# Optimization experiments

Hardware: AMD Instinct MI355X
Metric: run time of the kernel (lower is better)

The kernel has to match this reference:

```python
import jax, jax.numpy as jnp
import numpy as np

NHEAD = 16  # n_head; head_size N = C // NHEAD = 64


def _forward(x, time_maa_x, time_maa, time_maa_w1, time_maa_w2,
             time_decay, time_decay_w1, time_decay_w2,
             time_aaaaa, time_aaa_w1, time_aaa_w2,
             time_kkk_w1, time_kkk_w2,
             gate_w1, gate_w2,
             time_misc_a, ma_w1, ma_w2,
             time_misc_k, mk_w1, mk_w2,
             receptance, key_w, value, output,
             ln_w, ln_b, time_faaaa):
    B, T, C = x.shape
    H, N = NHEAD, C // NHEAD
    # --- fused_time_shift: token shift + 4-way LoRA mixing (rg, wa, k, v) ---
    xprev = jnp.pad(x, ((0, 0), (1, 0), (0, 0)))[:, :T]   # shift right by one token
    xx = xprev - x
    xxx = x + xx * time_maa_x
    mix = jnp.tanh(xxx @ time_maa_w1.T).reshape(B, T, 4, -1)        # (B,T,4,32)
    deltas = jnp.einsum('btfd,fcd->fbtc', mix, time_maa_w2)         # (4,B,T,C)
    xrg, xwa, xk, xv = x[None] + xx[None] * (time_maa + deltas)
    # --- projections + small LoRAs ---
    r = xrg @ receptance.T
    g = jnp.tanh(xrg @ gate_w1.T) @ gate_w2.T                       # gate
    k = xk @ key_w.T
    kk1 = jnp.tanh(xk @ time_kkk_w1.T)
    mk1 = xk @ mk_w1.T
    v = xv @ value.T
    w1 = jnp.tanh(xwa @ time_decay_w1.T)
    a1 = xwa @ time_aaa_w1.T
    ma1 = xwa @ ma_w1.T
    # data-dependent log-decay, clamped <= -0.5 via softplus
    w = -jax.nn.softplus(-(time_decay + w1 @ time_decay_w2.T)) - 0.5
    # removal key kk: per-head L2-normalized
    kk = k + kk1 @ time_kkk_w2.T
    kk = kk.reshape(B, T, H, N)
    kk = kk / jnp.maximum(jnp.linalg.norm(kk, axis=-1, keepdims=True), 1e-12)
    kk = kk.reshape(B, T, C)
    a = jax.nn.sigmoid(time_aaaaa + a1 @ time_aaa_w2.T)
    ma = jax.nn.sigmoid(time_misc_a + ma1 @ ma_w2.T)
    k = k * ma + k * a * (1 - ma)
    mk = jax.nn.sigmoid(time_misc_k + mk1 @ mk_w2.T)
    k = k * jnp.exp(w * mk)
    b = -kk * a
    # --- RWKV-7 linear-attention scan; state S: (B,H,N_value,N_key) ---
    def heads(z):
        return z.reshape(B, T, H, N).transpose(1, 0, 2, 3)          # (T,B,H,N)
    rh, wh, kh, vh, kkh, bh = map(heads, (r, w, k, v, kk, b))

    def step(S, inp):
        r_, w_, k_, v_, kk_, b_ = inp
        sab = jnp.einsum('bhvk,bhk->bhv', S, kk_)                   # S @ kk
        S = (S * jnp.exp(w_)[:, :, None, :]                         # diag decay on key dim
             + sab[..., None] * b_[:, :, None, :]                   # (S kk) b^T  (delta-rule removal)
             + v_[..., None] * k_[:, :, None, :])                   # v k^T
        y = jnp.einsum('bhvk,bhk->bhv', S, r_)
        return S, y

    S0 = jnp.zeros((B, H, N, N), x.dtype)
    _, y = jax.lax.scan(step, S0, (rh, wh, kh, vh, kkh, bh))
    y = y.transpose(1, 0, 2, 3)                                     # (B,T,H,N)
    # --- GroupNorm (H groups, eps=64e-5) + r.k bonus + gate (fused_attn_ln tail) ---
    mu = y.mean(-1, keepdims=True)
    var = ((y - mu) ** 2).mean(-1, keepdims=True)
    yn = (y - mu) / jnp.sqrt(var + 0.00064) * ln_w.reshape(H, N) + ln_b.reshape(H, N)
    r4 = r.reshape(B, T, H, N)
    k4 = k.reshape(B, T, H, N)
    v4 = v.reshape(B, T, H, N)
    bonus = (r4 * k4 * time_faaaa.reshape(H, N)).sum(-1, keepdims=True) * v4
    out = (yn + bonus).reshape(B, T, C) * g
    return out @ output.T


def setup_inputs() -> dict:
    key = jax.random.key(0)
    ks = iter(jax.random.split(key, 40))
    B, T, C = 2, 1024, 1024
    def n(shape, s=1.0):
        return jax.random.normal(next(ks), shape, jnp.float32) * s
    def u(shape, lo, hi):
        return jax.random.uniform(next(ks), shape, jnp.float32, lo, hi)
    d = {}
    d['x'] = n((B, T, C))
    d['time_maa_x'] = u((1, 1, C), 0.0, 1.0)
    d['time_maa'] = u((4, 1, 1, C), 0.0, 1.0)
    d['time_maa_w1'] = n((128, C), 0.02)
    d['time_maa_w2'] = n((4, C, 32), 0.05)
    d['time_decay'] = u((1, 1, C), -6.5, -1.5)
    d['time_decay_w1'] = n((64, C), 0.02)
    d['time_decay_w2'] = n((C, 64), 0.05)
    d['time_aaaaa'] = n((1, 1, C), 0.1)
    d['time_aaa_w1'] = n((16, C), 0.02)
    d['time_aaa_w2'] = n((C, 16), 0.05)
    d['time_kkk_w1'] = n((16, C), 0.02)
    d['time_kkk_w2'] = n((C, 16), 0.05)
    d['gate_w1'] = n((128, C), 0.05)
    d['gate_w2'] = n((C, 128), 0.05)
    d['time_misc_a'] = n((1, 1, C), 0.1)
    d['ma_w1'] = n((16, C), 0.02)
    d['ma_w2'] = n((C, 16), 0.05)
    d['time_misc_k'] = n((1, 1, C), 0.1)
    d['mk_w1'] = n((16, C), 0.02)
    d['mk_w2'] = n((C, 16), 0.05)
    s = 0.5 / C ** 0.5
    d['receptance'] = u((C, C), -s, s)
    d['key_w'] = u((C, C), -0.1 * s, 0.1 * s)
    d['value'] = u((C, C), -s, s)
    d['output'] = n((C, C), 0.02)
    d['ln_w'] = jnp.ones((C,), jnp.float32)
    d['ln_b'] = jnp.zeros((C,), jnp.float32)
    d['time_faaaa'] = n((C,), 0.1)
    return d


def reference(x, time_maa_x, time_maa, time_maa_w1, time_maa_w2,
              time_decay, time_decay_w1, time_decay_w2,
              time_aaaaa, time_aaa_w1, time_aaa_w2,
              time_kkk_w1, time_kkk_w2,
              gate_w1, gate_w2,
              time_misc_a, ma_w1, ma_w2,
              time_misc_k, mk_w1, mk_w2,
              receptance, key_w, value, output,
              ln_w, ln_b, time_faaaa):
    return _forward(x, time_maa_x, time_maa, time_maa_w1, time_maa_w2,
                    time_decay, time_decay_w1, time_decay_w2,
                    time_aaaaa, time_aaa_w1, time_aaa_w2,
                    time_kkk_w1, time_kkk_w2,
                    gate_w1, gate_w2,
                    time_misc_a, ma_w1, ma_w2,
                    time_misc_k, mk_w1, mk_w2,
                    receptance, key_w, value, output,
                    ln_w, ln_b, time_faaaa)
```

## Files before the change

kernel.cpp:

```cpp
#include <hip/hip_runtime.h>
#include <hip/hip_bf16.h>

typedef __hip_bfloat16 bf16;

#define B_ 2
#define T_ 1024
#define C_ 1024
#define H_ 16
#define N_ 64

using short4v = __attribute__((ext_vector_type(4))) short;
using short8 = __attribute__((ext_vector_type(8))) short;
using f32x4 = __attribute__((ext_vector_type(4))) float;

__device__ __forceinline__ float bs2f(short s) {
  return __uint_as_float(((unsigned int)(unsigned short)s) << 16);
}
__device__ __forceinline__ bf16 f2bf(float f) { return __float2bfloat16(f); }
__device__ __forceinline__ short bfbits(float f) {
  bf16 h = __float2bfloat16(f);
  return *reinterpret_cast<short*>(&h);
}
__device__ __forceinline__ float sigmoidf_(float x) { return 1.0f / (1.0f + expf(-x)); }
__device__ __forceinline__ float softplusf_(float x) {
  return fmaxf(x, 0.0f) + log1pf(expf(-fabsf(x)));
}
__device__ __forceinline__ void gload16(const bf16* g, bf16* l) {
  __builtin_amdgcn_global_load_lds(
      (const __attribute__((address_space(1))) unsigned int*)g,
      (__attribute__((address_space(3))) unsigned int*)l, 16, 0, 0);
}
__device__ __forceinline__ float qsum16(float x) {
  int a = __builtin_amdgcn_update_dpp(0, __float_as_int(x), 0xB1, 0xF, 0xF, true);
  x += __int_as_float(a);
  int b = __builtin_amdgcn_update_dpp(0, __float_as_int(x), 0x4E, 0xF, 0xF, true);
  x += __int_as_float(b);
  int c = __builtin_amdgcn_update_dpp(0, __float_as_int(x), 0x124, 0xF, 0xF, true);
  x += __int_as_float(c);
  int d = __builtin_amdgcn_update_dpp(0, __float_as_int(x), 0x128, 0xF, 0xF, true);
  x += __int_as_float(d);
  return x;
}
__device__ __forceinline__ void qsum16x2(float& x, float& y) {
  int a0 = __builtin_amdgcn_update_dpp(0, __float_as_int(x), 0xB1, 0xF, 0xF, true);
  int b0 = __builtin_amdgcn_update_dpp(0, __float_as_int(y), 0xB1, 0xF, 0xF, true);
  x += __int_as_float(a0); y += __int_as_float(b0);
  int a1 = __builtin_amdgcn_update_dpp(0, __float_as_int(x), 0x4E, 0xF, 0xF, true);
  int b1 = __builtin_amdgcn_update_dpp(0, __float_as_int(y), 0x4E, 0xF, 0xF, true);
  x += __int_as_float(a1); y += __int_as_float(b1);
  int a2 = __builtin_amdgcn_update_dpp(0, __float_as_int(x), 0x124, 0xF, 0xF, true);
  int b2 = __builtin_amdgcn_update_dpp(0, __float_as_int(y), 0x124, 0xF, 0xF, true);
  x += __int_as_float(a2); y += __int_as_float(b2);
  int a3 = __builtin_amdgcn_update_dpp(0, __float_as_int(x), 0x128, 0xF, 0xF, true);
  int b3 = __builtin_amdgcn_update_dpp(0, __float_as_int(y), 0x128, 0xF, 0xF, true);
  x += __int_as_float(a3); y += __int_as_float(b3);
}

__global__ __launch_bounds__(256) void cvt_mix_kernel(
    const float* __restrict__ s0, const float* __restrict__ s1,
    const float* __restrict__ s2, const float* __restrict__ s3,
    const float* __restrict__ s4, const float* __restrict__ s5,
    const float* __restrict__ s6,
    bf16* __restrict__ d0, bf16* __restrict__ d1, bf16* __restrict__ d2w,
    bf16* __restrict__ d3, bf16* __restrict__ d4, bf16* __restrict__ d5,
    bf16* __restrict__ d6,
    const float* __restrict__ tkw1, const float* __restrict__ mkw1,
    const float* __restrict__ tdw1, const float* __restrict__ taw1,
    const float* __restrict__ maw1,
    bf16* __restrict__ wsk, bf16* __restrict__ wswa,
    const float* __restrict__ tmw2, const float* __restrict__ tdw2,
    const float* __restrict__ tkw2, const float* __restrict__ taw2,
    const float* __restrict__ maw2, const float* __restrict__ mkw2,
    bf16* __restrict__ tmw2e, bf16* __restrict__ w2e5,
    const float* __restrict__ x, const float* __restrict__ tmx,
    bf16* __restrict__ mixb) {
  long bidx = blockIdx.x;
  if (bidx >= 5760) {
    __shared__ __align__(16) bf16 As[128][72];
    __shared__ __align__(16) bf16 Ws[64][72];
    const int K = 1024;
    int mb = (int)(bidx - 5760);
    int n0 = (mb & 1) << 6;
    int m0 = (mb >> 1) << 7;
    int tid = threadIdx.x;
    int arow = tid >> 1, acol = (tid & 1) << 5;
    int wrow = tid >> 2, wcol = (tid & 3) << 4;
    int wv = tid >> 6, lane = tid & 63;
    int fr = lane & 15, fq = lane >> 4;
    int grow = m0 + arow;
    int t = grow & (T_ - 1);
    const float* xp = x + (long)grow * C_ + acol;
    const float* Wp = s0 + (long)(n0 + wrow) * K + wcol;
    f32x4 a00 = {0.f, 0.f, 0.f, 0.f};
    f32x4 a01 = a00, a02 = a00, a03 = a00, a10 = a00, a11 = a00, a12 = a00, a13 = a00;
    for (int k0 = 0; k0 < K; k0 += 64) {
#pragma unroll
      for (int jj = 0; jj < 4; jj++) {
        int co = k0 + (jj << 3);
        float4 c0 = *(const float4*)(xp + co);
        float4 c1 = *(const float4*)(xp + co + 4);
        float4 q0 = {0.f, 0.f, 0.f, 0.f}, q1 = q0;
        if (t > 0) {
          q0 = *(const float4*)(xp + co - C_);
          q1 = *(const float4*)(xp + co + 4 - C_);
        }
        float4 m0v = *(const float4*)(tmx + co + acol);
        float4 m1v = *(const float4*)(tmx + co + acol + 4);
        short8 sv;
        sv[0] = bfbits(fmaf(q0.x - c0.x, m0v.x, c0.x));
        sv[1] = bfbits(fmaf(q0.y - c0.y, m0v.y, c0.y));
        sv[2] = bfbits(fmaf(q0.z - c0.z, m0v.z, c0.z));
        sv[3] = bfbits(fmaf(q0.w - c0.w, m0v.w, c0.w));
        sv[4] = bfbits(fmaf(q1.x - c1.x, m1v.x, c1.x));
        sv[5] = bfbits(fmaf(q1.y - c1.y, m1v.y, c1.y));
        sv[6] = bfbits(fmaf(q1.z - c1.z, m1v.z, c1.z));
        sv[7] = bfbits(fmaf(q1.w - c1.w, m1v.w, c1.w));
        *(short8*)&As[arow][acol + (jj << 3)] = sv;
      }
      {
        float4 w0 = *(const float4*)(Wp + k0);
        float4 w1 = *(const float4*)(Wp + k0 + 4);
        float4 w2 = *(const float4*)(Wp + k0 + 8);
        float4 w3 = *(const float4*)(Wp + k0 + 12);
        short8 wv0, wv1;
        wv0[0] = bfbits(w0.x); wv0[1] = bfbits(w0.y); wv0[2] = bfbits(w0.z); wv0[3] = bfbits(w0.w);
        wv0[4] = bfbits(w1.x); wv0[5] = bfbits(w1.y); wv0[6] = bfbits(w1.z); wv0[7] = bfbits(w1.w);
        wv1[0] = bfbits(w2.x); wv1[1] = bfbits(w2.y); wv1[2] = bfbits(w2.z); wv1[3] = bfbits(w2.w);
        wv1[4] = bfbits(w3.x); wv1[5] = bfbits(w3.y); wv1[6] = bfbits(w3.z); wv1[7] = bfbits(w3.w);
        *(short8*)&Ws[wrow][wcol] = wv0;
        *(short8*)&Ws[wrow][wcol + 8] = wv1;
      }
      __syncthreads();
#pragma unroll
      for (int kk = 0; kk < 2; kk++) {
        int ko = (fq << 3) + (kk << 5);
        short8 af0 = *(const short8*)&As[(wv << 5) + fr][ko];
        short8 af1 = *(const short8*)&As[(wv << 5) + 16 + fr][ko];
        short8 b0 = *(const short8*)&Ws[fr][ko];
        short8 b1 = *(const short8*)&Ws[16 + fr][ko];
        short8 b2 = *(const short8*)&Ws[32 + fr][ko];
        short8 b3 = *(const short8*)&Ws[48 + fr][ko];
        a00 = __builtin_amdgcn_mfma_f32_16x16x32_bf16(af0, b0, a00, 0, 0, 0);
        a01 = __builtin_amdgcn_mfma_f32_16x16x32_bf16(af0, b1, a01, 0, 0, 0);
        a02 = __builtin_amdgcn_mfma_f32_16x16x32_bf16(af0, b2, a02, 0, 0, 0);
        a03 = __builtin_amdgcn_mfma_f32_16x16x32_bf16(af0, b3, a03, 0, 0, 0);
        a10 = __builtin_amdgcn_mfma_f32_16x16x32_bf16(af1, b0, a10, 0, 0, 0);
        a11 = __builtin_amdgcn_mfma_f32_16x16x32_bf16(af1, b1, a11, 0, 0, 0);
        a12 = __builtin_amdgcn_mfma_f32_16x16x32_bf16(af1, b2, a12, 0, 0, 0);
        a13 = __builtin_amdgcn_mfma_f32_16x16x32_bf16(af1, b3, a13, 0, 0, 0);
      }
      __syncthreads();
    }
    const int Nz = 128;
    int ocol = n0 + fr;
    int orow0 = m0 + (wv << 5) + (fq << 2);
#define WRM(accv, mf, nt) { int col = ocol + ((nt) << 4); \
    _Pragma("unroll") for (int r = 0; r < 4; r++) { \
      long oi = (long)(orow0 + ((mf) << 4) + r) * Nz + col; \
      mixb[oi] = f2bf(tanhf(accv[r])); } }
    WRM(a00, 0, 0) WRM(a01, 0, 1) WRM(a02, 0, 2) WRM(a03, 0, 3)
    WRM(a10, 1, 0) WRM(a11, 1, 1) WRM(a12, 1, 2) WRM(a13, 1, 3)
#undef WRM
    return;
  }
  const float* s; bf16* d; long off;
  if (bidx < 4480) {
    long i4 = bidx * 256 + threadIdx.x;
    if (i4 < 32768) { s = s0; d = d0; off = i4; }
    else if (i4 < 294912) { s = s1; d = d1; off = i4 - 32768; }
    else if (i4 < 327680) { s = s2; d = d2w; off = i4 - 294912; }
    else if (i4 < 360448) { s = s3; d = d3; off = i4 - 327680; }
    else if (i4 < 622592) { s = s4; d = d4; off = i4 - 360448; }
    else if (i4 < 884736) { s = s5; d = d5; off = i4 - 622592; }
    else { s = s6; d = d6; off = i4 - 884736; }
  } else if (bidx < 4608) {
    long i4 = (bidx - 4480) * 256 + threadIdx.x;
    long so, dof;
    if (i4 < 4096) { s = tkw1; so = i4; d = wsk; dof = i4; }
    else if (i4 < 8192) { s = mkw1; so = i4 - 4096; d = wsk; dof = i4; }
    else if (i4 < 24576) { s = tdw1; so = i4 - 8192; d = wswa; dof = i4 - 8192; }
    else if (i4 < 28672) { s = taw1; so = i4 - 24576; d = wswa; dof = i4 - 8192; }
    else { s = maw1; so = i4 - 28672; d = wswa; dof = i4 - 8192; }
    float4 v = *(const float4*)(s + so * 4);
    d[dof * 4 + 0] = f2bf(v.x); d[dof * 4 + 1] = f2bf(v.y);
    d[dof * 4 + 2] = f2bf(v.z); d[dof * 4 + 3] = f2bf(v.w);
    return;
  } else if (bidx < 5120) {
    long i4 = (bidx - 4608) * 256 + threadIdx.x;
    long n = i4 >> 5;
    int k0 = (int)(i4 & 31) << 2;
    int f = (int)(n >> 10);
    float4 v = {0.f, 0.f, 0.f, 0.f};
    if ((k0 >> 5) == f) v = *(const float4*)(tmw2 + n * 32 + (k0 & 31));
    tmw2e[i4 * 4 + 0] = f2bf(v.x);
    tmw2e[i4 * 4 + 1] = f2bf(v.y);
    tmw2e[i4 * 4 + 2] = f2bf(v.z);
    tmw2e[i4 * 4 + 3] = f2bf(v.w);
    return;
  } else {
    long i4 = (bidx - 5120) * 256 + threadIdx.x;
    long rowi = i4 >> 5;
    int k0 = (int)(i4 & 31) << 2;
    int j = (int)(rowi >> 10);
    int c = (int)(rowi & 1023);
    float4 v = {0.f, 0.f, 0.f, 0.f};
    if (j == 0) { if (k0 < 64) v = *(const float4*)(tdw2 + c * 64 + k0); }
    else if (j == 1) { if (k0 >= 64 && k0 < 80) v = *(const float4*)(taw2 + c * 16 + (k0 - 64)); }
    else if (j == 2) { if (k0 >= 80 && k0 < 96) v = *(const float4*)(maw2 + c * 16 + (k0 - 80)); }
    else if (j == 3) { if (k0 >= 96 && k0 < 112) v = *(const float4*)(tkw2 + c * 16 + (k0 - 96)); }
    else { if (k0 >= 112) v = *(const float4*)(mkw2 + c * 16 + (k0 - 112)); }
    w2e5[i4 * 4 + 0] = f2bf(v.x);
    w2e5[i4 * 4 + 1] = f2bf(v.y);
    w2e5[i4 * 4 + 2] = f2bf(v.z);
    w2e5[i4 * 4 + 3] = f2bf(v.w);
    return;
  }
  float4 v = *(const float4*)(s + off * 4);
  d[off * 4 + 0] = f2bf(v.x);
  d[off * 4 + 1] = f2bf(v.y);
  d[off * 4 + 2] = f2bf(v.z);
  d[off * 4 + 3] = f2bf(v.w);
}

struct GemmBatch {
  const bf16* A[6]; const bf16* W[6];
  float* Cf[6]; bf16* Cb[6];
  int N[6]; int actN[6]; int ldc[6]; int coff[6];
};

__global__ __launch_bounds__(256) void gemm_batch_kernel(GemmBatch gb, int K) {
  __shared__ __align__(16) bf16 As[128][64];
  __shared__ __align__(16) bf16 Ws[64][64];
  int z = blockIdx.z;
  int Nz = gb.N[z];
  int n0 = blockIdx.x << 6;
  if (n0 >= Nz) return;
  int m0 = blockIdx.y << 7;
  int actN = gb.actN[z];
  int ldc = gb.ldc[z], coff = gb.coff[z];
  const bf16* A = gb.A[z];
  const bf16* W = gb.W[z];
  float* Cf = gb.Cf[z];
  bf16* Cb = gb.Cb[z];
  int tid = threadIdx.x;
  int wrow = tid >> 2, wcol = (tid & 3) << 4;
  int wv = tid >> 6, lane = tid & 63;
  int fr = lane & 15, fq = lane >> 4;
  int lrow = lane >> 3, lcol = (lane & 7) << 3;
  bool wok = (n0 + wrow) < Nz;
  bool fullW = (n0 + 64 <= Nz);
  const bf16* Ag = A + (long)m0 * K;
  const bf16* Wg = W + (long)n0 * K;
  const bf16* Wp = W + (long)(n0 + wrow) * K + wcol;
  short8 zz = {0, 0, 0, 0, 0, 0, 0, 0};
  f32x4 a00 = {0.f, 0.f, 0.f, 0.f};
  f32x4 a01 = a00, a02 = a00, a03 = a00, a10 = a00, a11 = a00, a12 = a00, a13 = a00;
  for (int k0 = 0; k0 < K; k0 += 64) {
#pragma unroll
    for (int i = 0; i < 4; i++) {
      int rb = (wv << 5) + (i << 3);
      gload16(Ag + (long)(rb + lrow) * K + k0 + lcol, &As[rb][0]);
    }
    if (fullW) {
#pragma unroll
      for (int i = 0; i < 2; i++) {
        int rb = (wv << 4) + (i << 3);
        gload16(Wg + (long)(rb + lrow) * K + k0 + lcol, &Ws[rb][0]);
      }
    } else {
      *(short8*)&Ws[wrow][wcol] = wok ? *(const short8*)(Wp + k0) : zz;
      *(short8*)&Ws[wrow][wcol + 8] = wok ? *(const short8*)(Wp + k0 + 8) : zz;
    }
    __syncthreads();
#pragma unroll
    for (int kk = 0; kk < 2; kk++) {
      int ko = (fq << 3) + (kk << 5);
      short8 af0 = *(const short8*)&As[(wv << 5) + fr][ko];
      short8 af1 = *(const short8*)&As[(wv << 5) + 16 + fr][ko];
      short8 b0 = *(const short8*)&Ws[fr][ko];
      short8 b1 = *(const short8*)&Ws[16 + fr][ko];
      short8 b2 = *(const short8*)&Ws[32 + fr][ko];
      short8 b3 = *(const short8*)&Ws[48 + fr][ko];
      a00 = __builtin_amdgcn_mfma_f32_16x16x32_bf16(af0, b0, a00, 0, 0, 0);
      a01 = __builtin_amdgcn_mfma_f32_16x16x32_bf16(af0, b1, a01, 0, 0, 0);
      a02 = __builtin_amdgcn_mfma_f32_16x16x32_bf16(af0, b2, a02, 0, 0, 0);
      a03 = __builtin_amdgcn_mfma_f32_16x16x32_bf16(af0, b3, a03, 0, 0, 0);
      a10 = __builtin_amdgcn_mfma_f32_16x16x32_bf16(af1, b0, a10, 0, 0, 0);
      a11 = __builtin_amdgcn_mfma_f32_16x16x32_bf16(af1, b1, a11, 0, 0, 0);
      a12 = __builtin_amdgcn_mfma_f32_16x16x32_bf16(af1, b2, a12, 0, 0, 0);
      a13 = __builtin_amdgcn_mfma_f32_16x16x32_bf16(af1, b3, a13, 0, 0, 0);
    }
    __syncthreads();
  }
  int ocol = n0 + fr;
  int orow0 = m0 + (wv << 5) + (fq << 2);
#define WRB(accv, mf, nt) { int col = ocol + ((nt) << 4); if (col < Nz) { \
    _Pragma("unroll") for (int r = 0; r < 4; r++) { \
      float vvv = accv[r]; if (col < actN) vvv = tanhf(vvv); \
      long oi = (long)(orow0 + ((mf) << 4) + r) * ldc + coff + col; \
      if (Cb) Cb[oi] = f2bf(vvv); else Cf[oi] = vvv; } } }
  WRB(a00, 0, 0) WRB(a01, 0, 1) WRB(a02, 0, 2) WRB(a03, 0, 3)
  WRB(a10, 1, 0) WRB(a11, 1, 1) WRB(a12, 1, 2) WRB(a13, 1, 3)
#undef WRB
}

__global__ __launch_bounds__(256) void gemm_mixapply_kernel(
    const bf16* __restrict__ A, const bf16* __restrict__ W,
    const float* __restrict__ x, const float* __restrict__ tmaa,
    bf16* __restrict__ xrg, bf16* __restrict__ xwa,
    bf16* __restrict__ xk, bf16* __restrict__ xv) {
  __shared__ __align__(16) bf16 As[128][64];
  __shared__ __align__(16) bf16 Ws[64][64];
  const int K = 128;
  int n0 = blockIdx.x << 6;
  int m0 = blockIdx.y << 7;
  int tid = threadIdx.x;
  int wv = tid >> 6, lane = tid & 63;
  int fr = lane & 15, fq = lane >> 4;
  int lrow = lane >> 3, lcol = (lane & 7) << 3;
  const bf16* Ag = A + (long)m0 * K;
  const bf16* Wg = W + (long)n0 * K;
  f32x4 a00 = {0.f, 0.f, 0.f, 0.f};
  f32x4 a01 = a00, a02 = a00, a03 = a00, a10 = a00, a11 = a00, a12 = a00, a13 = a00;
  for (int k0 = 0; k0 < K; k0 += 64) {
#pragma unroll
    for (int i = 0; i < 4; i++) {
      int rb = (wv << 5) + (i << 3);
      gload16(Ag + (long)(rb + lrow) * K + k0 + lcol, &As[rb][0]);
    }
#pragma unroll
    for (int i = 0; i < 2; i++) {
      int rb = (wv << 4) + (i << 3);
      gload16(Wg + (long)(rb + lrow) * K + k0 + lcol, &Ws[rb][0]);
    }
    __syncthreads();
#pragma unroll
    for (int kk = 0; kk < 2; kk++) {
      int ko = (fq << 3) + (kk << 5);
      short8 af0 = *(const short8*)&As[(wv << 5) + fr][ko];
      short8 af1 = *(const short8*)&As[(wv << 5) + 16 + fr][ko];
      short8 b0 = *(const short8*)&Ws[fr][ko];
      short8 b1 = *(const short8*)&Ws[16 + fr][ko];
      short8 b2 = *(const short8*)&Ws[32 + fr][ko];
      short8 b3 = *(const short8*)&Ws[48 + fr][ko];
      a00 = __builtin_amdgcn_mfma_f32_16x16x32_bf16(af0, b0, a00, 0, 0, 0);
      a01 = __builtin_amdgcn_mfma_f32_16x16x32_bf16(af0, b1, a01, 0, 0, 0);
      a02 = __builtin_amdgcn_mfma_f32_16x16x32_bf16(af0, b2, a02, 0, 0, 0);
      a03 = __builtin_amdgcn_mfma_f32_16x16x32_bf16(af0, b3, a03, 0, 0, 0);
      a10 = __builtin_amdgcn_mfma_f32_16x16x32_bf16(af1, b0, a10, 0, 0, 0);
      a11 = __builtin_amdgcn_mfma_f32_16x16x32_bf16(af1, b1, a11, 0, 0, 0);
      a12 = __builtin_amdgcn_mfma_f32_16x16x32_bf16(af1, b2, a12, 0, 0, 0);
      a13 = __builtin_amdgcn_mfma_f32_16x16x32_bf16(af1, b3, a13, 0, 0, 0);
    }
    __syncthreads();
  }
  int f = n0 >> 10;
  int c0 = n0 & 1023;
  bf16* outp = (f == 0) ? xrg : (f == 1) ? xwa : (f == 2) ? xk : xv;
  int ocol = c0 + fr;
  int orow0 = m0 + (wv << 5) + (fq << 2);
#define WRA(accv, mf, nt) { int cc = ocol + ((nt) << 4); \
    float ta = tmaa[(f << 10) + cc]; \
    _Pragma("unroll") for (int r = 0; r < 4; r++) { \
      int row = orow0 + ((mf) << 4) + r; \
      int t = row & (T_ - 1); \
      long xo = (long)row * C_ + cc; \
      float xb = x[xo]; \
      float xq = (t > 0) ? x[xo - C_] : 0.0f; \
      outp[xo] = f2bf(fmaf(xq - xb, ta + accv[r], xb)); } }
  WRA(a00, 0, 0) WRA(a01, 0, 1) WRA(a02, 0, 2) WRA(a03, 0, 3)
  WRA(a10, 1, 0) WRA(a11, 1, 1) WRA(a12, 1, 2) WRA(a13, 1, 3)
#undef WRA
}

__global__ __launch_bounds__(256) void fuse2_kernel(
    const float* __restrict__ kraw, const float* __restrict__ d2,
    const float* __restrict__ tdec, const float* __restrict__ taa,
    const float* __restrict__ tma, const float* __restrict__ tmk,
    float* __restrict__ ew, float* __restrict__ kfin,
    float* __restrict__ kkn, float* __restrict__ bbo) {
  int m = blockIdx.x, tid = threadIdx.x;
  int c4 = tid << 2;
  const float* dp = d2 + (long)m * 5120;
  float4 wd4 = *(const float4*)(dp + c4);
  float4 ad4 = *(const float4*)(dp + 1024 + c4);
  float4 mad4 = *(const float4*)(dp + 2048 + c4);
  float4 kd4 = *(const float4*)(dp + 3072 + c4);
  float4 mkd4 = *(const float4*)(dp + 4096 + c4);
  float4 kraw4 = *(const float4*)(kraw + (long)m * C_ + c4);
  float4 tdec4 = *(const float4*)(tdec + c4);
  float4 taa4 = *(const float4*)(taa + c4);
  float4 tma4 = *(const float4*)(tma + c4);
  float4 tmk4 = *(const float4*)(tmk + c4);
  float wd[4] = {wd4.x, wd4.y, wd4.z, wd4.w};
  float ad[4] = {ad4.x, ad4.y, ad4.z, ad4.w};
  float mad[4] = {mad4.x, mad4.y, mad4.z, mad4.w};
  float kd[4] = {kd4.x, kd4.y, kd4.z, kd4.w};
  float mkd[4] = {mkd4.x, mkd4.y, mkd4.z, mkd4.w};
  float krw[4] = {kraw4.x, kraw4.y, kraw4.z, kraw4.w};
  float td[4] = {tdec4.x, tdec4.y, tdec4.z, tdec4.w};
  float ta[4] = {taa4.x, taa4.y, taa4.z, taa4.w};
  float tm[4] = {tma4.x, tma4.y, tma4.z, tma4.w};
  float tk[4] = {tmk4.x, tmk4.y, tmk4.z, tmk4.w};
  float kkp[4], av[4], wvv[4], kr[4], mkv[4];
  float sumsq = 0.f;
#pragma unroll
  for (int j = 0; j < 4; j++) {
    float w = -softplusf_(-(td[j] + wd[j])) - 0.5f;
    wvv[j] = w;
    float kkpre = krw[j] + kd[j];
    kkp[j] = kkpre;
    sumsq += kkpre * kkpre;
    float a = sigmoidf_(ta[j] + ad[j]);
    av[j] = a;
    float ma = sigmoidf_(tm[j] + mad[j]);
    float mk = sigmoidf_(tk[j] + mkd[j]);
    mkv[j] = mk;
    kr[j] = krw[j] * (ma + a * (1.f - ma));
  }
  sumsq += __shfl_xor(sumsq, 1);
  sumsq += __shfl_xor(sumsq, 2);
  sumsq += __shfl_xor(sumsq, 4);
  sumsq += __shfl_xor(sumsq, 8);
  float rn = 1.0f / fmaxf(sqrtf(sumsq), 1e-12f);
  float4 kknv, bbov, eww, kfv;
  float* kknp = (float*)&kknv;
  float* bbop = (float*)&bbov;
  float* ewp = (float*)&eww;
  float* kfp = (float*)&kfv;
#pragma unroll
  for (int j = 0; j < 4; j++) {
    float kkx = kkp[j] * rn;
    kknp[j] = kkx;
    bbop[j] = -kkx * av[j];
    ewp[j] = expf(wvv[j]);
    kfp[j] = kr[j] * expf(wvv[j] * mkv[j]);
  }
  long off4 = (long)m * C_ + c4;
  *(float4*)(kkn + off4) = kknv;
  *(float4*)(bbo + off4) = bbov;
  *(float4*)(ew + off4) = eww;
  *(float4*)(kfin + off4) = kfv;
}

#define SCHUNK 16
#define NCHUNK (T_ / SCHUNK)
__global__ __launch_bounds__(256, 1) void scan_kernel(
    const float* __restrict__ rB, const float* __restrict__ ewB,
    const float* __restrict__ kB, const float* __restrict__ vB,
    const float* __restrict__ kkB, const float* __restrict__ bbB,
    float* __restrict__ yB) {
  __shared__ __align__(16) float lds[2][6][SCHUNK * 64];
  int bid = blockIdx.x;
  int bh = bid >> 2, rg = bid & 3;
  int b = bh >> 4, h = bh & 15;
  int tid = threadIdx.x;
  int wave = tid >> 6, lane = tid & 63;
  int g = lane >> 4, q = lane & 15;
  int row = (rg << 4) + (wave << 2) + g;
  int kq = q << 2;
  const long base = ((long)b * T_) * C_ + (h << 6);
  const float* s0 = kkB + base;
  const float* s1 = ewB + base;
  const float* s2 = kB + base;
  const float* s3 = bbB + base;
  const float* s4 = rB + base;
  const float* s5 = vB + base;
  int stok = tid >> 4;
  int spc = (tid & 15) << 2;
  int lo = (stok << 6) + spc;
  float4 rb0, rb1, rb2, rb3, rb4, rb5;
  auto loadc = [&](int c) {
    long go = (long)((c << 4) + stok) * C_ + spc;
    rb0 = *(const float4*)(s0 + go);
    rb1 = *(const float4*)(s1 + go);
    rb2 = *(const float4*)(s2 + go);
    rb3 = *(const float4*)(s3 + go);
    rb4 = *(const float4*)(s4 + go);
    rb5 = *(const float4*)(s5 + go);
  };
  auto stage = [&](int buf) {
    *(float4*)&lds[buf][0][lo] = rb0;
    *(float4*)&lds[buf][1][lo] = rb1;
    *(float4*)&lds[buf][2][lo] = rb2;
    *(float4*)&lds[buf][3][lo] = rb3;
    *(float4*)&lds[buf][4][lo] = rb4;
    *(float4*)&lds[buf][5][lo] = rb5;
  };
  float S0 = 0.f, S1 = 0.f, S2 = 0.f, S3 = 0.f;
  float ypv = 0.f;
  float4 Q0kk, Q0ew, Q0k, Q0bb, Q0r; float Q0v;
  float4 Q1kk, Q1ew, Q1k, Q1bb, Q1r; float Q1v;
  float4 Q2kk, Q2ew, Q2k, Q2bb, Q2r; float Q2v;

#define PF(i, tt) { int tb_ = ((tt) << 6); \
    Q##i##kk = *(const float4*)&lds[cur][0][tb_ + kq]; \
    Q##i##ew = *(const float4*)&lds[cur][1][tb_ + kq]; \
    Q##i##k  = *(const float4*)&lds[cur][2][tb_ + kq]; \
    Q##i##bb = *(const float4*)&lds[cur][3][tb_ + kq]; \
    Q##i##r  = *(const float4*)&lds[cur][4][tb_ + kq]; \
    Q##i##v  = lds[cur][5][tb_ + row]; }
#define SBAR __builtin_amdgcn_sched_barrier(0x7)
#define ST(i, gtok, FIRSTT) { \
    float p_ = fmaf(S1, Q##i##kk.y, S0 * Q##i##kk.x) + \
               fmaf(S3, Q##i##kk.w, S2 * Q##i##kk.z); \
    float yo_ = ypv; \
    qsum16x2(p_, yo_); \
    if (q == 0 && !((FIRSTT) && c == 0)) \
      yB[base + (long)((gtok) - 1) * C_ + row] = yo_; \
    float n0 = fmaf(S0, Q##i##ew.x, Q##i##v * Q##i##k.x); \
    float n1 = fmaf(S1, Q##i##ew.y, Q##i##v * Q##i##k.y); \
    float n2 = fmaf(S2, Q##i##ew.z, Q##i##v * Q##i##k.z); \
    float n3 = fmaf(S3, Q##i##ew.w, Q##i##v * Q##i##k.w); \
    S0 = fmaf(p_, Q##i##bb.x, n0); \
    S1 = fmaf(p_, Q##i##bb.y, n1); \
    S2 = fmaf(p_, Q##i##bb.z, n2); \
    S3 = fmaf(p_, Q##i##bb.w, n3); \
    ypv = fmaf(S1, Q##i##r.y, S0 * Q##i##r.x) + \
          fmaf(S3, Q##i##r.w, S2 * Q##i##r.z); }

  loadc(0);
  stage(0);
  loadc(1);
  __syncthreads();
  int cur = 0;
  for (int c = 0; c < NCHUNK; c++) {
    int t0 = c << 4;
    PF(0, 0); PF(1, 1);
    if (c + 1 < NCHUNK) stage(cur ^ 1);
    if (c + 2 < NCHUNK) loadc(c + 2);
    SBAR;
    PF(2, 2);  SBAR; ST(0, t0 + 0, true);
    PF(0, 3);  SBAR; ST(1, t0 + 1, false);
    PF(1, 4);  SBAR; ST(2, t0 + 2, false);
    PF(2, 5);  SBAR; ST(0, t0 + 3, false);
    PF(0, 6);  SBAR; ST(1, t0 + 4, false);
    PF(1, 7);  SBAR; ST(2, t0 + 5, false);
    PF(2, 8);  SBAR; ST(0, t0 + 6, false);
    PF(0, 9);  SBAR; ST(1, t0 + 7, false);
    PF(1, 10); SBAR; ST(2, t0 + 8, false);
    PF(2, 11); SBAR; ST(0, t0 + 9, false);
    PF(0, 12); SBAR; ST(1, t0 + 10, false);
    PF(1, 13); SBAR; ST(2, t0 + 11, false);
    PF(2, 14); SBAR; ST(0, t0 + 12, false);
    PF(0, 15); SBAR; ST(1, t0 + 13, false);
    ST(2, t0 + 14, false);
    ST(0, t0 + 15, false);
    __syncthreads();
    cur ^= 1;
  }
  {
    float yo = qsum16(ypv);
    if (q == 0) yB[base + (long)(T_ - 1) * C_ + row] = yo;
  }
#undef PF
#undef SBAR
#undef ST
}

__global__ __launch_bounds__(256) void gnout_kernel(
    const float* __restrict__ y, const float* __restrict__ r,
    const float* __restrict__ kf, const float* __restrict__ v,
    const float* __restrict__ g,
    const float* __restrict__ lnw, const float* __restrict__ lnb,
    const float* __restrict__ fa, bf16* __restrict__ z) {
  int tid = threadIdx.x;
  int w = tid >> 6, lane = tid & 63;
  int gi = (blockIdx.x << 2) + w;
  int h = gi & 15, mt = gi >> 4;
  long off = (long)mt * C_ + (h << 6) + lane;
  float yv = y[off];
  float s = yv;
  s += __shfl_xor(s, 1); s += __shfl_xor(s, 2); s += __shfl_xor(s, 4);
  s += __shfl_xor(s, 8); s += __shfl_xor(s, 16); s += __shfl_xor(s, 32);
  float mu = s * (1.0f / 64.0f);
  float d = yv - mu;
  float s2 = d * d;
  s2 += __shfl_xor(s2, 1); s2 += __shfl_xor(s2, 2); s2 += __shfl_xor(s2, 4);
  s2 += __shfl_xor(s2, 8); s2 += __shfl_xor(s2, 16); s2 += __shfl_xor(s2, 32);
  float var = s2 * (1.0f / 64.0f);
  int hc = (h << 6) + lane;
  float dot = r[off] * kf[off] * fa[hc];
  dot += __shfl_xor(dot, 1); dot += __shfl_xor(dot, 2); dot += __shfl_xor(dot, 4);
  dot += __shfl_xor(dot, 8); dot += __shfl_xor(dot, 16); dot += __shfl_xor(dot, 32);
  float yn = d * rsqrtf(var + 0.00064f) * lnw[hc] + lnb[hc];
  z[off] = f2bf((yn + dot * v[off]) * g[off]);
}

extern "C" void kernel_launch(void* const* d_in, const int* in_sizes, int n_in,
                              void* d_out, int out_size, void* d_ws, size_t ws_size,
                              hipStream_t stream) {
  const float* x = (const float*)d_in[0];
  const float* tmx = (const float*)d_in[1];
  const float* tmaa = (const float*)d_in[2];
  const float* tmw1 = (const float*)d_in[3];
  const float* tmw2 = (const float*)d_in[4];
  const float* tdec = (const float*)d_in[5];
  const float* tdw1 = (const float*)d_in[6];
  const float* tdw2 = (const float*)d_in[7];
  const float* taa5 = (const float*)d_in[8];
  const float* taw1 = (const float*)d_in[9];
  const float* taw2 = (const float*)d_in[10];
  const float* tkw1 = (const float*)d_in[11];
  const float* tkw2 = (const float*)d_in[12];
  const float* gw1 = (const float*)d_in[13];
  const float* gw2 = (const float*)d_in[14];
  const float* tmia = (const float*)d_in[15];
  const float* maw1 = (const float*)d_in[16];
  const float* maw2 = (const float*)d_in[17];
  const float* tmik = (const float*)d_in[18];
  const float* mkw1 = (const float*)d_in[19];
  const float* mkw2 = (const float*)d_in[20];
  const float* wrec = (const float*)d_in[21];
  const float* wkey = (const float*)d_in[22];
  const float* wval = (const float*)d_in[23];
  const float* wout = (const float*)d_in[24];
  const float* lnw = (const float*)d_in[25];
  const float* lnb = (const float*)d_in[26];
  const float* faaa = (const float*)d_in[27];

  const long MT = 2048, CC = 1024;
  char* base = (char*)d_ws;
  float* y = (float*)base;     base += MT * CC * 4;
  bf16* xrgb = (bf16*)base;    base += MT * CC * 2;
  bf16* xwab = (bf16*)base;    base += MT * CC * 2;
  bf16* xkb = (bf16*)base;     base += MT * CC * 2;
  bf16* xvb = (bf16*)base;     base += MT * CC * 2;
  float* rr = (float*)base;    base += MT * CC * 4;
  float* kraw = (float*)base;  base += MT * CC * 4;
  float* vv = (float*)base;    base += MT * CC * 4;
  float* gg = (float*)base;    base += MT * CC * 4;
  float* bbo = (float*)base;   base += MT * CC * 4;
  bf16* g1b = (bf16*)base;     base += MT * 128 * 2;
  bf16* out12b = (bf16*)base;  base += MT * 128 * 2;
  bf16* zb = (bf16*)base;      base += MT * CC * 2;
  bf16* mixb = (bf16*)base;    base += MT * 128 * 2;
  float* d2 = (float*)base;    base += MT * 5120L * 4;
  bf16* tmw1b = (bf16*)base;   base += 128 * CC * 2;
  bf16* wrecb = (bf16*)base;   base += CC * CC * 2;
  bf16* gw1b = (bf16*)base;    base += 128 * CC * 2;
  bf16* gw2b = (bf16*)base;    base += CC * 128 * 2;
  bf16* wkeyb = (bf16*)base;   base += CC * CC * 2;
  bf16* wvalb = (bf16*)base;   base += CC * CC * 2;
  bf16* woutb = (bf16*)base;   base += CC * CC * 2;
  bf16* wskb = (bf16*)base;    base += 32 * CC * 2;
  bf16* wswab = (bf16*)base;   base += 96 * CC * 2;
  bf16* tmw2e = (bf16*)base;   base += 4096L * 128 * 2;
  bf16* w2e5b = (bf16*)base;   base += 5120L * 128 * 2;
  float* ew = kraw;
  float* kfin = (float*)xrgb;
  float* kkn = (float*)xkb;

  cvt_mix_kernel<<<5792, 256, 0, stream>>>(
      tmw1, wrec, gw1, gw2, wkey, wval, wout,
      tmw1b, wrecb, gw1b, gw2b, wkeyb, wvalb, woutb,
      tkw1, mkw1, tdw1, taw1, maw1, wskb, wswab,
      tmw2, tdw2, tkw2, taw2, maw2, mkw2,
      tmw2e, w2e5b, x, tmx, mixb);

  gemm_mixapply_kernel<<<dim3(64, 16), 256, 0, stream>>>(
      mixb, tmw2e, x, tmaa, xrgb, xwab, xkb, xvb);
  {
    GemmBatch gb = {};
    gb.A[0] = xrgb; gb.W[0] = wrecb; gb.Cf[0] = rr;      gb.Cb[0] = nullptr; gb.N[0] = 1024; gb.actN[0] = 0;   gb.ldc[0] = 1024; gb.coff[0] = 0;
    gb.A[1] = xrgb; gb.W[1] = gw1b;  gb.Cf[1] = nullptr; gb.Cb[1] = g1b;     gb.N[1] = 128;  gb.actN[1] = 128; gb.ldc[1] = 128;  gb.coff[1] = 0;
    gb.A[2] = xkb;  gb.W[2] = wkeyb; gb.Cf[2] = kraw;    gb.Cb[2] = nullptr; gb.N[2] = 1024; gb.actN[2] = 0;   gb.ldc[2] = 1024; gb.coff[2] = 0;
    gb.A[3] = xkb;  gb.W[3] = wskb;  gb.Cf[3] = nullptr; gb.Cb[3] = out12b;  gb.N[3] = 32;   gb.actN[3] = 16;  gb.ldc[3] = 128;  gb.coff[3] = 96;
    gb.A[4] = xvb;  gb.W[4] = wvalb; gb.Cf[4] = vv;      gb.Cb[4] = nullptr; gb.N[4] = 1024; gb.actN[4] = 0;   gb.ldc[4] = 1024; gb.coff[4] = 0;
    gb.A[5] = xwab; gb.W[5] = wswab; gb.Cf[5] = nullptr; gb.Cb[5] = out12b;  gb.N[5] = 96;   gb.actN[5] = 64;  gb.ldc[5] = 128;  gb.coff[5] = 0;
    gemm_batch_kernel<<<dim3(16, 16, 6), 256, 0, stream>>>(gb, 1024);
  }
  {
    GemmBatch gb = {};
    gb.A[0] = g1b;    gb.W[0] = gw2b;  gb.Cf[0] = gg; gb.Cb[0] = nullptr; gb.N[0] = 1024; gb.actN[0] = 0; gb.ldc[0] = 1024; gb.coff[0] = 0;
    gb.A[1] = out12b; gb.W[1] = w2e5b; gb.Cf[1] = d2; gb.Cb[1] = nullptr; gb.N[1] = 5120; gb.actN[1] = 0; gb.ldc[1] = 5120; gb.coff[1] = 0;
    gemm_batch_kernel<<<dim3(80, 16, 2), 256, 0, stream>>>(gb, 128);
  }
  fuse2_kernel<<<2048, 256, 0, stream>>>(kraw, d2, tdec, taa5, tmia, tmik,
                                         ew, kfin, kkn, bbo);
  scan_kernel<<<128, 256, 0, stream>>>(rr, ew, kfin, vv, kkn, bbo, y);
  gnout_kernel<<<8192, 256, 0, stream>>>(y, rr, kfin, vv, gg, lnw, lnb, faaa, zb);
  {
    GemmBatch gb = {};
    gb.A[0] = zb; gb.W[0] = woutb; gb.Cf[0] = (float*)d_out; gb.Cb[0] = nullptr;
    gb.N[0] = 1024; gb.actN[0] = 0; gb.ldc[0] = 1024; gb.coff[0] = 0;
    gemm_batch_kernel<<<dim3(16, 16, 1), 256, 0, stream>>>(gb, 1024);
  }
}
```

Baseline: 423.4 us.

## Merge mid-pipeline GEMMs and fuse2 into one persistent cooperative kernel

Turns the mix-apply GEMM, the batched projection GEMMs, the LoRA second-stage GEMMs and the fuse2 elementwise pass into device functions. A single cooperative kernel walks over virtual block indices for each stage, with grid.sync between stages. The aim is to remove kernel launch gaps and tail idle time between the four launches. In exchange, it adds grid-wide barriers, caps the grid at occupancy×256 persistent blocks, and replaces the former z-indexed batching with an explicit tile-index map.

```diff
diff --git a/kernel.cpp b/kernel.cpp
--- a/kernel.cpp
+++ b/kernel.cpp
@@ -1,5 +1,8 @@
 #include <hip/hip_runtime.h>
 #include <hip/hip_bf16.h>
+#include <hip/hip_cooperative_groups.h>
+
+namespace cg = cooperative_groups;
 
 typedef __hip_bfloat16 bf16;
 
@@ -222,26 +225,10 @@
   d[off * 4 + 3] = f2bf(v.w);
 }
 
-struct GemmBatch {
-  const bf16* A[6]; const bf16* W[6];
-  float* Cf[6]; bf16* Cb[6];
-  int N[6]; int actN[6]; int ldc[6]; int coff[6];
-};
-
-__global__ __launch_bounds__(256) void gemm_batch_kernel(GemmBatch gb, int K) {
-  __shared__ __align__(16) bf16 As[128][64];
-  __shared__ __align__(16) bf16 Ws[64][64];
-  int z = blockIdx.z;
-  int Nz = gb.N[z];
-  int n0 = blockIdx.x << 6;
-  if (n0 >= Nz) return;
-  int m0 = blockIdx.y << 7;
-  int actN = gb.actN[z];
-  int ldc = gb.ldc[z], coff = gb.coff[z];
-  const bf16* A = gb.A[z];
-  const bf16* W = gb.W[z];
-  float* Cf = gb.Cf[z];
-  bf16* Cb = gb.Cb[z];
+__device__ __forceinline__ void gemm_tile(
+    const bf16* __restrict__ A, const bf16* __restrict__ W,
+    float* Cf, bf16* Cb, int Nz, int actN, int ldc, int coff, int K,
+    int n0, int m0, bf16* As, bf16* Ws) {
   int tid = threadIdx.x;
   int wrow = tid >> 2, wcol = (tid & 3) << 4;
   int wv = tid >> 6, lane = tid & 63;
@@ -259,28 +246,28 @@
 #pragma unroll
     for (int i = 0; i < 4; i++) {
       int rb = (wv << 5) + (i << 3);
-      gload16(Ag + (long)(rb + lrow) * K + k0 + lcol, &As[rb][0]);
+      gload16(Ag + (long)(rb + lrow) * K + k0 + lcol, As + rb * 64);
     }
     if (fullW) {
 #pragma unroll
       for (int i = 0; i < 2; i++) {
         int rb = (wv << 4) + (i << 3);
-        gload16(Wg + (long)(rb + lrow) * K + k0 + lcol, &Ws[rb][0]);
+        gload16(Wg + (long)(rb + lrow) * K + k0 + lcol, Ws + rb * 64);
       }
     } else {
-      *(short8*)&Ws[wrow][wcol] = wok ? *(const short8*)(Wp + k0) : zz;
-      *(short8*)&Ws[wrow][wcol + 8] = wok ? *(const short8*)(Wp + k0 + 8) : zz;
+      *(short8*)(Ws + wrow * 64 + wcol) = wok ? *(const short8*)(Wp + k0) : zz;
+      *(short8*)(Ws + wrow * 64 + wcol + 8) = wok ? *(const short8*)(Wp + k0 + 8) : zz;
     }
     __syncthreads();
 #pragma unroll
     for (int kk = 0; kk < 2; kk++) {
       int ko = (fq << 3) + (kk << 5);
-      short8 af0 = *(const short8*)&As[(wv << 5) + fr][ko];
-      short8 af1 = *(const short8*)&As[(wv << 5) + 16 + fr][ko];
-      short8 b0 = *(const short8*)&Ws[fr][ko];
-      short8 b1 = *(const short8*)&Ws[16 + fr][ko];
-      short8 b2 = *(const short8*)&Ws[32 + fr][ko];
-      short8 b3 = *(const short8*)&Ws[48 + fr][ko];
+      short8 af0 = *(const short8*)(As + ((wv << 5) + fr) * 64 + ko);
+      short8 af1 = *(const short8*)(As + ((wv << 5) + 16 + fr) * 64 + ko);
+      short8 b0 = *(const short8*)(Ws + fr * 64 + ko);
+      short8 b1 = *(const short8*)(Ws + (16 + fr) * 64 + ko);
+      short8 b2 = *(const short8*)(Ws + (32 + fr) * 64 + ko);
+      short8 b3 = *(const short8*)(Ws + (48 + fr) * 64 + ko);
       a00 = __builtin_amdgcn_mfma_f32_16x16x32_bf16(af0, b0, a00, 0, 0, 0);
       a01 = __builtin_amdgcn_mfma_f32_16x16x32_bf16(af0, b1, a01, 0, 0, 0);
       a02 = __builtin_amdgcn_mfma_f32_16x16x32_bf16(af0, b2, a02, 0, 0, 0);
@@ -304,16 +291,12 @@
 #undef WRB
 }
 
-__global__ __launch_bounds__(256) void gemm_mixapply_kernel(
+__device__ __forceinline__ void mixapply_tile(
     const bf16* __restrict__ A, const bf16* __restrict__ W,
     const float* __restrict__ x, const float* __restrict__ tmaa,
-    bf16* __restrict__ xrg, bf16* __restrict__ xwa,
-    bf16* __restrict__ xk, bf16* __restrict__ xv) {
-  __shared__ __align__(16) bf16 As[128][64];
-  __shared__ __align__(16) bf16 Ws[64][64];
+    bf16* xrg, bf16* xwa, bf16* xk, bf16* xv,
+    int n0, int m0, bf16* As, bf16* Ws) {
   const int K = 128;
-  int n0 = blockIdx.x << 6;
-  int m0 = blockIdx.y << 7;
   int tid = threadIdx.x;
   int wv = tid >> 6, lane = tid & 63;
   int fr = lane & 15, fq = lane >> 4;
@@ -326,23 +309,23 @@
 #pragma unroll
     for (int i = 0; i < 4; i++) {
       int rb = (wv << 5) + (i << 3);
-      gload16(Ag + (long)(rb + lrow) * K + k0 + lcol, &As[rb][0]);
+      gload16(Ag + (long)(rb + lrow) * K + k0 + lcol, As + rb * 64);
     }
 #pragma unroll
     for (int i = 0; i < 2; i++) {
       int rb = (wv << 4) + (i << 3);
-      gload16(Wg + (long)(rb + lrow) * K + k0 + lcol, &Ws[rb][0]);
+      gload16(Wg + (long)(rb + lrow) * K + k0 + lcol, Ws + rb * 64);
     }
     __syncthreads();
 #pragma unroll
     for (int kk = 0; kk < 2; kk++) {
       int ko = (fq << 3) + (kk << 5);
-      short8 af0 = *(const short8*)&As[(wv << 5) + fr][ko];
-      short8 af1 = *(const short8*)&As[(wv << 5) + 16 + fr][ko];
-      short8 b0 = *(const short8*)&Ws[fr][ko];
-      short8 b1 = *(const short8*)&Ws[16 + fr][ko];
-      short8 b2 = *(const short8*)&Ws[32 + fr][ko];
-      short8 b3 = *(const short8*)&Ws[48 + fr][ko];
+      short8 af0 = *(const short8*)(As + ((wv << 5) + fr) * 64 + ko);
+      short8 af1 = *(const short8*)(As + ((wv << 5) + 16 + fr) * 64 + ko);
+      short8 b0 = *(const short8*)(Ws + fr * 64 + ko);
+      short8 b1 = *(const short8*)(Ws + (16 + fr) * 64 + ko);
+      short8 b2 = *(const short8*)(Ws + (32 + fr) * 64 + ko);
+      short8 b3 = *(const short8*)(Ws + (48 + fr) * 64 + ko);
       a00 = __builtin_amdgcn_mfma_f32_16x16x32_bf16(af0, b0, a00, 0, 0, 0);
       a01 = __builtin_amdgcn_mfma_f32_16x16x32_bf16(af0, b1, a01, 0, 0, 0);
       a02 = __builtin_amdgcn_mfma_f32_16x16x32_bf16(af0, b2, a02, 0, 0, 0);
@@ -373,13 +356,12 @@
 #undef WRA
 }
 
-__global__ __launch_bounds__(256) void fuse2_kernel(
+__device__ __forceinline__ void fuse2_body(
     const float* __restrict__ kraw, const float* __restrict__ d2,
     const float* __restrict__ tdec, const float* __restrict__ taa,
     const float* __restrict__ tma, const float* __restrict__ tmk,
-    float* __restrict__ ew, float* __restrict__ kfin,
-    float* __restrict__ kkn, float* __restrict__ bbo) {
-  int m = blockIdx.x, tid = threadIdx.x;
+    float* ew, float* kfin, float* kkn, float* bbo, int m) {
+  int tid = threadIdx.x;
   int c4 = tid << 2;
   const float* dp = d2 + (long)m * 5120;
   float4 wd4 = *(const float4*)(dp + c4);
@@ -441,6 +423,71 @@
   *(float4*)(bbo + off4) = bbov;
   *(float4*)(ew + off4) = eww;
   *(float4*)(kfin + off4) = kfv;
+}
+
+struct MidArgs {
+  const bf16 *mixb, *tmw2e;
+  const float *x, *tmaa;
+  bf16 *xrgb, *xwab, *xkb, *xvb;
+  const bf16 *wrecb, *gw1b, *wkeyb, *wskb, *wvalb, *wswab;
+  float *rr, *kraw, *vv;
+  bf16 *g1b, *out12b;
+  const bf16 *gw2b, *w2e5b;
+  float *gg, *d2;
+  const float *tdec, *taa, *tma, *tmk;
+  float *ew, *kfin, *kkn, *bbo;
+};
+
+__global__ __launch_bounds__(256, 4) void mid_coop_kernel(MidArgs a) {
+  __shared__ __align__(16) bf16 smem[128 * 64 + 64 * 64];
+  bf16* As = smem;
+  bf16* Ws = smem + 128 * 64;
+  cg::grid_group grid = cg::this_grid();
+  int nb = gridDim.x;
+  for (int vb = blockIdx.x; vb < 1024; vb += nb) {
+    int n0 = (vb & 63) << 6;
+    int m0 = (vb >> 6) << 7;
+    mixapply_tile(a.mixb, a.tmw2e, a.x, a.tmaa, a.xrgb, a.xwab, a.xkb, a.xvb,
+                  n0, m0, As, Ws);
+  }
+  grid.sync();
+  for (int vb = blockIdx.x; vb < 848; vb += nb) {
+    const bf16 *A, *W; float* Cf = nullptr; bf16* Cb = nullptr;
+    int Nz, actN, ldc, coff, nx, rem;
+    if (vb < 256)      { rem = vb;       nx = 16; A = a.xrgb; W = a.wrecb; Cf = a.rr;     Nz = 1024; actN = 0;   ldc = 1024; coff = 0;  }
+    else if (vb < 288) { rem = vb - 256; nx = 2;  A = a.xrgb; W = a.gw1b;  Cb = a.g1b;    Nz = 128;  actN = 128; ldc = 128;  coff = 0;  }
+    else if (vb < 544) { rem = vb - 288; nx = 16; A = a.xkb;  W = a.wkeyb; Cf = a.kraw;   Nz = 1024; actN = 0;   ldc = 1024; coff = 0;  }
+    else if (vb < 560) { rem = vb - 544; nx = 1;  A = a.xkb;  W = a.wskb;  Cb = a.out12b; Nz = 32;   actN = 16;  ldc = 128;  coff = 96; }
+    else if (vb < 816) { rem = vb - 560; nx = 16; A = a.xvb;  W = a.wvalb; Cf = a.vv;     Nz = 1024; actN = 0;   ldc = 1024; coff = 0;  }
+    else               { rem = vb - 816; nx = 2;  A = a.xwab; W = a.wswab; Cb = a.out12b; Nz = 96;   actN = 64;  ldc = 128;  coff = 0;  }
+    int n0 = (rem % nx) << 6;
+    int m0 = (rem / nx) << 7;
+    gemm_tile(A, W, Cf, Cb, Nz, actN, ldc, coff, 1024, n0, m0, As, Ws);
+  }
+  grid.sync();
+  for (int vb = blockIdx.x; vb < 1536; vb += nb) {
+    if (vb < 256) {
+      int n0 = (vb & 15) << 6, m0 = (vb >> 4) << 7;
+      gemm_tile(a.g1b, a.gw2b, a.gg, nullptr, 1024, 0, 1024, 0, 128, n0, m0, As, Ws);
+    } else {
+      int rem = vb - 256;
+      int n0 = (rem % 80) << 6, m0 = (rem / 80) << 7;
+      gemm_tile(a.out12b, a.w2e5b, a.d2, nullptr, 5120, 0, 5120, 0, 128, n0, m0, As, Ws);
+    }
+  }
+  grid.sync();
+  for (int m = blockIdx.x; m < 2048; m += nb) {
+    fuse2_body(a.kraw, a.d2, a.tdec, a.taa, a.tma, a.tmk,
+               a.ew, a.kfin, a.kkn, a.bbo, m);
+  }
+}
+
+__global__ __launch_bounds__(256) void gemm_out_kernel(
+    const bf16* __restrict__ A, const bf16* __restrict__ W,
+    float* __restrict__ C) {
+  __shared__ __align__(16) bf16 smem[128 * 64 + 64 * 64];
+  gemm_tile(A, W, C, nullptr, 1024, 0, 1024, 0, 1024,
+            blockIdx.x << 6, blockIdx.y << 7, smem, smem + 128 * 64);
 }
 
 #define SCHUNK 16
@@ -658,32 +705,29 @@
       tmw2, tdw2, tkw2, taw2, maw2, mkw2,
       tmw2e, w2e5b, x, tmx, mixb);
 
-  gemm_mixapply_kernel<<<dim3(64, 16), 256, 0, stream>>>(
-      mixb, tmw2e, x, tmaa, xrgb, xwab, xkb, xvb);
   {
-    GemmBatch gb = {};
-    gb.A[0] = xrgb; gb.W[0] = wrecb; gb.Cf[0] = rr;      gb.Cb[0] = nullptr; gb.N[0] = 1024; gb.actN[0] = 0;   gb.ldc[0] = 1024; gb.coff[0] = 0;
-    gb.A[1] = xrgb; gb.W[1] = gw1b;  gb.Cf[1] = nullptr; gb.Cb[1] = g1b;     gb.N[1] = 128;  gb.actN[1] = 128; gb.ldc[1] = 128;  gb.coff[1] = 0;
-    gb.A[2] = xkb;  gb.W[2] = wkeyb; gb.Cf[2] = kraw;    gb.Cb[2] = nullptr; gb.N[2] = 1024; gb.actN[2] = 0;   gb.ldc[2] = 1024; gb.coff[2] = 0;
-    gb.A[3] = xkb;  gb.W[3] = wskb;  gb.Cf[3] = nullptr; gb.Cb[3] = out12b;  gb.N[3] = 32;   gb.actN[3] = 16;  gb.ldc[3] = 128;  gb.coff[3] = 96;
-    gb.A[4] = xvb;  gb.W[4] = wvalb; gb.Cf[4] = vv;      gb.Cb[4] = nullptr; gb.N[4] = 1024; gb.actN[4] = 0;   gb.ldc[4] = 1024; gb.coff[4] = 0;
-    gb.A[5] = xwab; gb.W[5] = wswab; gb.Cf[5] = nullptr; gb.Cb[5] = out12b;  gb.N[5] = 96;   gb.actN[5] = 64;  gb.ldc[5] = 128;  gb.coff[5] = 0;
-    gemm_batch_kernel<<<dim3(16, 16, 6), 256, 0, stream>>>(gb, 1024);
-  }
-  {
-    GemmBatch gb = {};
-    gb.A[0] = g1b;    gb.W[0] = gw2b;  gb.Cf[0] = gg; gb.Cb[0] = nullptr; gb.N[0] = 1024; gb.actN[0] = 0; gb.ldc[0] = 1024; gb.coff[0] = 0;
-    gb.A[1] = out12b; gb.W[1] = w2e5b; gb.Cf[1] = d2; gb.Cb[1] = nullptr; gb.N[1] = 5120; gb.actN[1] = 0; gb.ldc[1] = 5120; gb.coff[1] = 0;
-    gemm_batch_kernel<<<dim3(80, 16, 2), 256, 0, stream>>>(gb, 128);
-  }
-  fuse2_kernel<<<2048, 256, 0, stream>>>(kraw, d2, tdec, taa5, tmia, tmik,
-                                         ew, kfin, kkn, bbo);
+    MidArgs ma;
+    ma.mixb = mixb; ma.tmw2e = tmw2e; ma.x = x; ma.tmaa = tmaa;
+    ma.xrgb = xrgb; ma.xwab = xwab; ma.xkb = xkb; ma.xvb = xvb;
+    ma.wrecb = wrecb; ma.gw1b = gw1b; ma.wkeyb = wkeyb; ma.wskb = wskb;
+    ma.wvalb = wvalb; ma.wswab = wswab;
+    ma.rr = rr; ma.kraw = kraw; ma.vv = vv;
+    ma.g1b = g1b; ma.out12b = out12b;
+    ma.gw2b = gw2b; ma.w2e5b = w2e5b;
+    ma.gg = gg; ma.d2 = d2;
+    ma.tdec = tdec; ma.taa = taa5; ma.tma = tmia; ma.tmk = tmik;
+    ma.ew = ew; ma.kfin = kfin; ma.kkn = kkn; ma.bbo = bbo;
+    int maxb = 0;
+    hipOccupancyMaxActiveBlocksPerMultiprocessor(&maxb, mid_coop_kernel, 256, 0);
+    if (maxb < 1) maxb = 1;
+    int grid = maxb * 256;
+    if (grid > 1024) grid = 1024;
+    void* kargs[] = {&ma};
+    hipLaunchCooperativeKernel((void*)mid_coop_kernel, dim3(grid), dim3(256),
+                               kargs, 0, stream);
+  }
+
   scan_kernel<<<128, 256, 0, stream>>>(rr, ew, kfin, vv, kkn, bbo, y);
   gnout_kernel<<<8192, 256, 0, stream>>>(y, rr, kfin, vv, gg, lnw, lnb, faaa, zb);
-  {
-    GemmBatch gb = {};
-    gb.A[0] = zb; gb.W[0] = woutb; gb.Cf[0] = (float*)d_out; gb.Cb[0] = nullptr;
-    gb.N[0] = 1024; gb.actN[0] = 0; gb.ldc[0] = 1024; gb.coff[0] = 0;
-    gemm_batch_kernel<<<dim3(16, 16, 1), 256, 0, stream>>>(gb, 1024);
-  }
-}
+  gemm_out_kernel<<<dim3(16, 16), 256, 0, stream>>>(zb, woutb, (float*)d_out);
+}
```

After: 644.3 us. +52.2%, slower.
